# Kernel tuning notes

Hardware: AMD Instinct MI355X
Metric: run time of the kernel (lower is better)

## Reference

```python
import jax, jax.numpy as jnp
import numpy as np

LATENT = 256
HIDDEN = 512
NODE_F = 128
MAX_NODES = 50
B = 128


def _mk_linear(key, fan_in, fan_out):
    kw, kb = jax.random.split(key)
    bound = 1.0 / np.sqrt(fan_in)
    W = jax.random.uniform(kw, (fan_in, fan_out), jnp.float32, -bound, bound)
    b = jax.random.uniform(kb, (fan_out,), jnp.float32, -bound, bound)
    return W, b


def setup_inputs() -> dict:
    key = jax.random.key(0)
    ks = jax.random.split(key, 7)
    z = jax.random.normal(ks[0], (B, LATENT), jnp.float32)
    # node decoder: latent -> hidden -> hidden -> max_nodes*node_features
    nw1, nb1 = _mk_linear(ks[1], LATENT, HIDDEN)
    nw2, nb2 = _mk_linear(ks[2], HIDDEN, HIDDEN)
    nw3, nb3 = _mk_linear(ks[3], HIDDEN, MAX_NODES * NODE_F)
    # edge decoder: latent + 2*node_features -> hidden -> hidden//2 -> 1
    ew1, eb1 = _mk_linear(ks[4], LATENT + 2 * NODE_F, HIDDEN)
    ew2, eb2 = _mk_linear(ks[5], HIDDEN, HIDDEN // 2)
    ew3, eb3 = _mk_linear(ks[6], HIDDEN // 2, 1)
    return {"z": z,
            "nw1": nw1, "nb1": nb1, "nw2": nw2, "nb2": nb2, "nw3": nw3, "nb3": nb3,
            "ew1": ew1, "eb1": eb1, "ew2": ew2, "eb2": eb2, "ew3": ew3, "eb3": eb3}


def reference(z, nw1, nb1, nw2, nb2, nw3, nb3, ew1, eb1, ew2, eb2, ew3, eb3):
    # ---- node decoder ----
    h = jax.nn.relu(z @ nw1 + nb1)
    h = jax.nn.relu(h @ nw2 + nb2)
    node_logits = h @ nw3 + nb3                      # [B, MAX_NODES*NODE_F]
    node_feats = node_logits.reshape(z.shape[0], MAX_NODES, NODE_F)
    node_probs = jax.nn.sigmoid(node_feats)

    # ---- edge decoder: vectorize the O(N^2) python loop over upper-tri pairs ----
    # jnp.triu_indices matches the torch loop order: i ascending, j ascending per i.
    ii, jj = jnp.triu_indices(MAX_NODES, k=1)        # [P] each, P = 1225
    ni = node_feats[:, ii, :]                        # [B, P, NODE_F]
    nj = node_feats[:, jj, :]                        # [B, P, NODE_F]
    zb = jnp.broadcast_to(z[:, None, :], (z.shape[0], ii.shape[0], z.shape[1]))
    edge_in = jnp.concatenate([zb, ni, nj], axis=-1)  # [B, P, LATENT+2*NODE_F]
    e = jax.nn.relu(edge_in @ ew1 + eb1)             # [B, P, HIDDEN]
    e = jax.nn.relu(e @ ew2 + eb2)                   # [B, P, HIDDEN//2]
    edge_probs = jax.nn.sigmoid(e @ ew3 + eb3)[..., 0]  # [B, P]
    return node_probs, edge_probs
```

## Files before the change

### kernel.cpp

```cpp
#include <hip/hip_runtime.h>
#include <hip/hip_bf16.h>
#include <math.h>

#define LATENT 256
#define HIDDEN 512
#define NODE_F 128
#define MAX_NODES 50
#define NPAIRS 1225
#define BATCH 128
#define NODE_OUT 6400
#define MTILE 64
#define TPB 10
#define NBLK 256

typedef __attribute__((ext_vector_type(8))) short short8;
typedef __attribute__((ext_vector_type(4))) float float4v;

union S8U { short8 s; unsigned int u[4]; };

__device__ __forceinline__ float bf2f(ushort u) {
    union { unsigned int i; float f; } v; v.i = ((unsigned int)u) << 16; return v.f;
}
__device__ __forceinline__ ushort f2bf(float f) {
    union { unsigned int i; float f; } v; v.f = f;
    unsigned int r = v.i + 0x7fffu + ((v.i >> 16) & 1u);
    return (ushort)(r >> 16);
}
__device__ __forceinline__ unsigned int pk_bf16(float f0, float f1) {
    __hip_bfloat162 p = __float22bfloat162_rn(float2{f0, f1});
    unsigned int w; __builtin_memcpy(&w, &p, 4); return w;
}
__device__ __forceinline__ float sigmoidf(float x) {
    return 1.0f / (1.0f + __expf(-x));
}

#define TR3_B0   0
#define EW2_B0   800
#define WIU_B0   832
#define WIV_B0   848
#define ZC_B0    864
#define ND_B0    1120
#define PT_B0    1376
#define PREPK_NB 1381

__global__ __launch_bounds__(256) void k_prep_all(
    const float* __restrict__ nw3, ushort* __restrict__ nw3T,
    const float* __restrict__ ew1, const float* __restrict__ ew2,
    ushort* __restrict__ ew2T, ushort* __restrict__ wijT,
    const float* __restrict__ z, const float* __restrict__ eb1,
    float* __restrict__ Zc,
    const float* __restrict__ nw1, const float* __restrict__ nb1,
    const float* __restrict__ nw2, const float* __restrict__ nb2,
    ushort* __restrict__ h2b, int* __restrict__ ptab)
{
    __shared__ float smem[64 * 65];
    int b = blockIdx.x;
    int tid = threadIdx.x;
    int tx = tid & 63, ty = tid >> 6;

    if (b < EW2_B0) {
        int bb = b - TR3_B0;
        int k0 = (bb & 7) * 64;
        int n0 = (bb >> 3) * 64;
#pragma unroll
        for (int r = 0; r < 16; r++) {
            int row = r * 4 + ty;
            smem[row * 65 + tx] = nw3[(k0 + row) * NODE_OUT + n0 + tx];
        }
        __syncthreads();
#pragma unroll
        for (int c = 0; c < 16; c++) {
            int n = c * 4 + ty;
            nw3T[(size_t)(n0 + n) * HIDDEN + k0 + tx] = f2bf(smem[tx * 65 + n]);
        }
    } else if (b < WIU_B0) {
        int bb = b - EW2_B0;
        int k0 = (bb >> 2) * 64;
        int n0 = (bb & 3) * 64;
#pragma unroll
        for (int r = 0; r < 16; r++) {
            int row = r * 4 + ty;
            smem[row * 65 + tx] = ew2[(k0 + row) * 256 + n0 + tx];
        }
        __syncthreads();
#pragma unroll
        for (int c = 0; c < 16; c++) {
            int n = c * 4 + ty;
            ew2T[(n0 + n) * HIDDEN + k0 + tx] = f2bf(smem[tx * 65 + n]);
        }
    } else if (b < WIV_B0) {
        int bb = b - WIU_B0;
        int k0 = (bb >> 3) * 64;
        int n0 = (bb & 7) * 64;
#pragma unroll
        for (int r = 0; r < 16; r++) {
            int row = r * 4 + ty;
            smem[row * 65 + tx] = ew1[(256 + k0 + row) * 512 + n0 + tx];
        }
        __syncthreads();
#pragma unroll
        for (int c = 0; c < 16; c++) {
            int n = c * 4 + ty;
            wijT[(n0 + n) * NODE_F + k0 + tx] = f2bf(smem[tx * 65 + n]);
        }
    } else if (b < ZC_B0) {
        int bb = b - WIV_B0;
        int k0 = (bb >> 3) * 64;
        int n0 = (bb & 7) * 64;
#pragma unroll
        for (int r = 0; r < 16; r++) {
            int row = r * 4 + ty;
            smem[row * 65 + tx] = ew1[(384 + k0 + row) * 512 + n0 + tx];
        }
        __syncthreads();
#pragma unroll
        for (int c = 0; c < 16; c++) {
            int n = c * 4 + ty;
            wijT[(512 + n0 + n) * NODE_F + k0 + tx] = f2bf(smem[tx * 65 + n]);
        }
    } else if (b < ND_B0) {
        int b2 = b - ZC_B0;
        int r = b2 >> 1, o = (b2 & 1) * 256 + tid;
        float* zs = smem;
        zs[tid] = z[r * LATENT + tid];
        __syncthreads();
        float acc = 0.f;
#pragma unroll 8
        for (int k = 0; k < LATENT; k++) acc += zs[k] * ew1[k * HIDDEN + o];
        Zc[r * HIDDEN + o] = acc + eb1[o];
    } else if (b < PT_B0) {
        int b2 = b - ND_B0;
        int r = b2 >> 1, half = b2 & 1;
        float* zs = smem;
        float* hs = smem + 256;
        zs[tid] = z[r * LATENT + tid];
        __syncthreads();
        float a0 = 0.f, a1 = 0.f;
#pragma unroll 8
        for (int k = 0; k < LATENT; k++) {
            float zk = zs[k];
            a0 += zk * nw1[k * HIDDEN + tid];
            a1 += zk * nw1[k * HIDDEN + tid + 256];
        }
        hs[tid]       = fmaxf(a0 + nb1[tid], 0.f);
        hs[tid + 256] = fmaxf(a1 + nb1[tid + 256], 0.f);
        __syncthreads();
        int o = half * 256 + tid;
        float acc = 0.f;
#pragma unroll 8
        for (int k = 0; k < HIDDEN; k++) acc += hs[k] * nw2[k * HIDDEN + o];
        acc += nb2[o];
        h2b[r * HIDDEN + o] = f2bf(fmaxf(acc, 0.f));
    } else {
        int p = (b - PT_B0) * 256 + tid;
        if (p < NPAIRS) {
            int i = 0, off = 0;
            while (p - off >= MAX_NODES - 1 - i) { off += MAX_NODES - 1 - i; ++i; }
            int j = i + 1 + (p - off);
            ptab[p] = (i << 8) | j;
        }
    }
}

__global__ __launch_bounds__(256, 4) void k_node_out_mfma(
    const ushort* __restrict__ h2b, const ushort* __restrict__ nw3T,
    const float* __restrict__ nb3, float* __restrict__ node_probs,
    ushort* __restrict__ node_feats)
{
    int tid = threadIdx.x;
    int wave = tid >> 6, lane = tid & 63;
    int m16 = lane & 15, quad = lane >> 4;
    int n0 = (blockIdx.x >> 1) * 64;
    int m0 = (blockIdx.x & 1) * 64;
    int col = n0 + wave * 16 + m16;

    float4v acc[4];
#pragma unroll
    for (int mt = 0; mt < 4; mt++) acc[mt] = (float4v)(0.f);

    const ushort* bb = nw3T + (size_t)col * HIDDEN;
#pragma unroll
    for (int it = 0; it < 16; ++it) {
        int kk = it * 32 + quad * 8;
        short8 b = *(const short8*)(bb + kk);
#pragma unroll
        for (int mt = 0; mt < 4; mt++) {
            short8 a = *(const short8*)(h2b + (m0 + mt * 16 + m16) * HIDDEN + kk);
            acc[mt] = __builtin_amdgcn_mfma_f32_16x16x32_bf16(a, b, acc[mt], 0, 0, 0);
        }
    }
    float bias = nb3[col];
#pragma unroll
    for (int mt = 0; mt < 4; mt++)
#pragma unroll
        for (int t = 0; t < 4; t++) {
            int row = m0 + mt * 16 + quad * 4 + t;
            float v = acc[mt][t] + bias;
            node_probs[(size_t)row * NODE_OUT + col] = sigmoidf(v);
            node_feats[(size_t)row * NODE_OUT + col] = f2bf(v);
        }
}

__global__ __launch_bounds__(256, 4) void k_uv(
    const ushort* __restrict__ nf, const ushort* __restrict__ wijT,
    ushort* __restrict__ UV)
{
    int tid = threadIdx.x;
    int wave = tid >> 6, lane = tid & 63;
    int m16 = lane & 15, quad = lane >> 4;
    int bm = blockIdx.x >> 2, bn = blockIdx.x & 3;
    int base = bn * 256 + wave * 64;
    int r0 = bm * 64;

    float4v acc[4][4];
#pragma unroll
    for (int mt = 0; mt < 4; mt++)
#pragma unroll
        for (int nt = 0; nt < 4; nt++) acc[mt][nt] = (float4v)(0.f);

#pragma unroll
    for (int k0 = 0; k0 < NODE_F; k0 += 32) {
        int kk = k0 + quad * 8;
        short8 a0 = *(const short8*)(nf + (r0 + m16) * NODE_F + kk);
        short8 a1 = *(const short8*)(nf + (r0 + 16 + m16) * NODE_F + kk);
        short8 a2 = *(const short8*)(nf + (r0 + 32 + m16) * NODE_F + kk);
        short8 a3 = *(const short8*)(nf + (r0 + 48 + m16) * NODE_F + kk);
#pragma unroll
        for (int nt = 0; nt < 4; nt++) {
            int n = base + nt * 16 + m16;
            short8 b = *(const short8*)(wijT + n * NODE_F + kk);
            acc[0][nt] = __builtin_amdgcn_mfma_f32_16x16x32_bf16(a0, b, acc[0][nt], 0, 0, 0);
            acc[1][nt] = __builtin_amdgcn_mfma_f32_16x16x32_bf16(a1, b, acc[1][nt], 0, 0, 0);
            acc[2][nt] = __builtin_amdgcn_mfma_f32_16x16x32_bf16(a2, b, acc[2][nt], 0, 0, 0);
            acc[3][nt] = __builtin_amdgcn_mfma_f32_16x16x32_bf16(a3, b, acc[3][nt], 0, 0, 0);
        }
    }
#pragma unroll
    for (int nt = 0; nt < 4; nt++) {
        int colg = base + nt * 16 + m16;
#pragma unroll
        for (int mt = 0; mt < 4; mt++)
#pragma unroll
            for (int t = 0; t < 4; t++) {
                int rr = r0 + mt * 16 + quad * 4 + t;
                UV[(size_t)rr * 1024 + colg] = f2bf(acc[mt][nt][t]);
            }
    }
}

__global__ __launch_bounds__(512, 2) void k_edge8(
    const float* __restrict__ Zc, const ushort* __restrict__ UV,
    const ushort* __restrict__ ew2T, const float* __restrict__ ew3,
    const float* __restrict__ eb2, const float* __restrict__ eb3,
    const int* __restrict__ ptab, float* __restrict__ out_edges)
{
    __shared__ __align__(16) ushort h1[2][MTILE][HIDDEN + 8];
    __shared__ float part[2][MTILE][33];
    __shared__ int uo5[TPB][MTILE], vo5[TPB][MTILE];

    int tid  = threadIdx.x;
    int blk  = blockIdx.x;
    int b    = blk >> 1;
    int ti0  = (blk & 1) * TPB;

    if (tid < MTILE) {
#pragma unroll
        for (int t = 0; t < TPB; t++) {
            int p = (ti0 + t) * MTILE + tid;
            if (p >= NPAIRS) p = NPAIRS - 1;
            int ij = ptab[p];
            uo5[t][tid] = (b * MAX_NODES + (ij >> 8)) * 1024;
            vo5[t][tid] = (b * MAX_NODES + (ij & 255)) * 1024 + 512;
        }
    }

    int wave = tid >> 6, lane = tid & 63;
    int m16 = lane & 15, quad = lane >> 4;
    int c8 = lane * 8;
    int kk0 = quad * 8;

    float4v zA = *(const float4v*)(Zc + b * HIDDEN + c8);
    float4v zB = *(const float4v*)(Zc + b * HIDDEN + c8 + 4);

    const ushort* bb0 = ew2T + (wave * 32 + m16) * HIDDEN;
    const ushort* bb1 = ew2T + (wave * 32 + 16 + m16) * HIDDEN;
    short8 Breg[16][2];
#pragma unroll
    for (int kc = 0; kc < 16; kc++) {
        Breg[kc][0] = *(const short8*)(bb0 + kc * 32 + kk0);
        Breg[kc][1] = *(const short8*)(bb1 + kc * 32 + kk0);
    }
    float eb2v[2], ew3v[2];
    eb2v[0] = eb2[wave * 32 + m16];      eb2v[1] = eb2[wave * 32 + 16 + m16];
    ew3v[0] = ew3[wave * 32 + m16];      ew3v[1] = ew3[wave * 32 + 16 + m16];

    __syncthreads();

#pragma unroll
    for (int rr = 0; rr < 8; rr++) {
        int r = wave * 8 + rr;
        short8 u8 = *(const short8*)(UV + uo5[0][r] + c8);
        short8 v8 = *(const short8*)(UV + vo5[0][r] + c8);
        S8U hh;
#pragma unroll
        for (int e2 = 0; e2 < 4; e2++) {
            float z0 = (e2 < 2) ? zA[e2 * 2] : zB[e2 * 2 - 4];
            float z1 = (e2 < 2) ? zA[e2 * 2 + 1] : zB[e2 * 2 - 3];
            float f0 = fmaxf(z0 + bf2f((ushort)u8[e2 * 2]) + bf2f((ushort)v8[e2 * 2]), 0.f);
            float f1 = fmaxf(z1 + bf2f((ushort)u8[e2 * 2 + 1]) + bf2f((ushort)v8[e2 * 2 + 1]), 0.f);
            hh.u[e2] = pk_bf16(f0, f1);
        }
        *(short8*)&h1[0][r][c8] = hh.s;
    }
    __syncthreads();

    for (int t = 0; t < TPB; t++) {
        int cur = t & 1, nxt = cur ^ 1;
        bool hasNext = (t + 1 < TPB);

        if (t > 0 && tid < MTILE) {
            int p = (ti0 + t - 1) * MTILE + tid;
            if (p < NPAIRS) {
                float v = eb3[0];
#pragma unroll
                for (int w = 0; w < 32; w++) v += part[nxt][tid][w];
                out_edges[b * NPAIRS + p] = sigmoidf(v);
            }
        }

        float4v acc2[4][2];
#pragma unroll
        for (int mt = 0; mt < 4; mt++)
#pragma unroll
            for (int nt = 0; nt < 2; nt++) acc2[mt][nt] = (float4v)(0.f);

        short8 uu[4], vv[4];
        if (hasNext) {
#pragma unroll
            for (int rr = 0; rr < 4; rr++) {
                int r = wave * 8 + rr;
                uu[rr] = *(const short8*)(UV + uo5[t + 1][r] + c8);
                vv[rr] = *(const short8*)(UV + vo5[t + 1][r] + c8);
            }
        }
#pragma unroll
        for (int it = 0; it < 8; ++it) {
            int kk = it * 32 + kk0;
            short8 a0 = *(const short8*)&h1[cur][m16][kk];
            short8 a1 = *(const short8*)&h1[cur][16 + m16][kk];
            short8 a2 = *(const short8*)&h1[cur][32 + m16][kk];
            short8 a3 = *(const short8*)&h1[cur][48 + m16][kk];
            acc2[0][0] = __builtin_amdgcn_mfma_f32_16x16x32_bf16(a0, Breg[it][0], acc2[0][0], 0, 0, 0);
            acc2[1][0] = __builtin_amdgcn_mfma_f32_16x16x32_bf16(a1, Breg[it][0], acc2[1][0], 0, 0, 0);
            acc2[2][0] = __builtin_amdgcn_mfma_f32_16x16x32_bf16(a2, Breg[it][0], acc2[2][0], 0, 0, 0);
            acc2[3][0] = __builtin_amdgcn_mfma_f32_16x16x32_bf16(a3, Breg[it][0], acc2[3][0], 0, 0, 0);
            acc2[0][1] = __builtin_amdgcn_mfma_f32_16x16x32_bf16(a0, Breg[it][1], acc2[0][1], 0, 0, 0);
            acc2[1][1] = __builtin_amdgcn_mfma_f32_16x16x32_bf16(a1, Breg[it][1], acc2[1][1], 0, 0, 0);
            acc2[2][1] = __builtin_amdgcn_mfma_f32_16x16x32_bf16(a2, Breg[it][1], acc2[2][1], 0, 0, 0);
            acc2[3][1] = __builtin_amdgcn_mfma_f32_16x16x32_bf16(a3, Breg[it][1], acc2[3][1], 0, 0, 0);
        }
        if (hasNext) {
#pragma unroll
            for (int rr = 0; rr < 4; rr++) {
                int r = wave * 8 + rr;
                S8U hh;
#pragma unroll
                for (int e2 = 0; e2 < 4; e2++) {
                    float z0 = (e2 < 2) ? zA[e2 * 2] : zB[e2 * 2 - 4];
                    float z1 = (e2 < 2) ? zA[e2 * 2 + 1] : zB[e2 * 2 - 3];
                    float f0 = fmaxf(z0 + bf2f((ushort)uu[rr][e2 * 2]) + bf2f((ushort)vv[rr][e2 * 2]), 0.f);
                    float f1 = fmaxf(z1 + bf2f((ushort)uu[rr][e2 * 2 + 1]) + bf2f((ushort)vv[rr][e2 * 2 + 1]), 0.f);
                    hh.u[e2] = pk_bf16(f0, f1);
                }
                *(short8*)&h1[nxt][r][c8] = hh.s;
            }
#pragma unroll
            for (int rr = 0; rr < 4; rr++) {
                int r = wave * 8 + 4 + rr;
                uu[rr] = *(const short8*)(UV + uo5[t + 1][r] + c8);
                vv[rr] = *(const short8*)(UV + vo5[t + 1][r] + c8);
            }
        }
#pragma unroll
        for (int it = 8; it < 16; ++it) {
            int kk = it * 32 + kk0;
            short8 a0 = *(const short8*)&h1[cur][m16][kk];
            short8 a1 = *(const short8*)&h1[cur][16 + m16][kk];
            short8 a2 = *(const short8*)&h1[cur][32 + m16][kk];
            short8 a3 = *(const short8*)&h1[cur][48 + m16][kk];
            acc2[0][0] = __builtin_amdgcn_mfma_f32_16x16x32_bf16(a0, Breg[it][0], acc2[0][0], 0, 0, 0);
            acc2[1][0] = __builtin_amdgcn_mfma_f32_16x16x32_bf16(a1, Breg[it][0], acc2[1][0], 0, 0, 0);
            acc2[2][0] = __builtin_amdgcn_mfma_f32_16x16x32_bf16(a2, Breg[it][0], acc2[2][0], 0, 0, 0);
            acc2[3][0] = __builtin_amdgcn_mfma_f32_16x16x32_bf16(a3, Breg[it][0], acc2[3][0], 0, 0, 0);
            acc2[0][1] = __builtin_amdgcn_mfma_f32_16x16x32_bf16(a0, Breg[it][1], acc2[0][1], 0, 0, 0);
            acc2[1][1] = __builtin_amdgcn_mfma_f32_16x16x32_bf16(a1, Breg[it][1], acc2[1][1], 0, 0, 0);
            acc2[2][1] = __builtin_amdgcn_mfma_f32_16x16x32_bf16(a2, Breg[it][1], acc2[2][1], 0, 0, 0);
            acc2[3][1] = __builtin_amdgcn_mfma_f32_16x16x32_bf16(a3, Breg[it][1], acc2[3][1], 0, 0, 0);
        }
        if (hasNext) {
#pragma unroll
            for (int rr = 0; rr < 4; rr++) {
                int r = wave * 8 + 4 + rr;
                S8U hh;
#pragma unroll
                for (int e2 = 0; e2 < 4; e2++) {
                    float z0 = (e2 < 2) ? zA[e2 * 2] : zB[e2 * 2 - 4];
                    float z1 = (e2 < 2) ? zA[e2 * 2 + 1] : zB[e2 * 2 - 3];
                    float f0 = fmaxf(z0 + bf2f((ushort)uu[rr][e2 * 2]) + bf2f((ushort)vv[rr][e2 * 2]), 0.f);
                    float f1 = fmaxf(z1 + bf2f((ushort)uu[rr][e2 * 2 + 1]) + bf2f((ushort)vv[rr][e2 * 2 + 1]), 0.f);
                    hh.u[e2] = pk_bf16(f0, f1);
                }
                *(short8*)&h1[nxt][r][c8] = hh.s;
            }
        }

#pragma unroll
        for (int mt = 0; mt < 4; mt++)
#pragma unroll
            for (int tt = 0; tt < 4; tt++) {
                float s = 0.f;
#pragma unroll
                for (int nt = 0; nt < 2; nt++)
                    s += fmaxf(acc2[mt][nt][tt] + eb2v[nt], 0.f) * ew3v[nt];
                s += __shfl_xor(s, 1);
                s += __shfl_xor(s, 2);
                if ((m16 & 3) == 0)
                    part[cur][mt * 16 + quad * 4 + tt][wave * 4 + (m16 >> 2)] = s;
            }
        __syncthreads();
    }

    if (tid < MTILE) {
        int p = (ti0 + TPB - 1) * MTILE + tid;
        if (p < NPAIRS) {
            float v = eb3[0];
#pragma unroll
            for (int w = 0; w < 32; w++) v += part[(TPB - 1) & 1][tid][w];
            out_edges[b * NPAIRS + p] = sigmoidf(v);
        }
    }
}

extern "C" void kernel_launch(void* const* d_in, const int* in_sizes, int n_in,
                              void* d_out, int out_size, void* d_ws, size_t ws_size,
                              hipStream_t stream) {
    const float* z   = (const float*)d_in[0];
    const float* nw1 = (const float*)d_in[1];
    const float* nb1 = (const float*)d_in[2];
    const float* nw2 = (const float*)d_in[3];
    const float* nb2 = (const float*)d_in[4];
    const float* nw3 = (const float*)d_in[5];
    const float* nb3 = (const float*)d_in[6];
    const float* ew1 = (const float*)d_in[7];
    const float* eb1 = (const float*)d_in[8];
    const float* ew2 = (const float*)d_in[9];
    const float* eb2 = (const float*)d_in[10];
    const float* ew3 = (const float*)d_in[11];
    const float* eb3 = (const float*)d_in[12];

    char* ws = (char*)d_ws;
    int*    ptab = (int*)(ws);
    ushort* h2b  = (ushort*)(ws + 262144);
    ushort* nf   = (ushort*)(ws + 393216);
    ushort* ew2T = (ushort*)(ws + 2031616);
    ushort* wijT = (ushort*)(ws + 2293760);
    ushort* nw3T = (ushort*)(ws + 2555904);
    float*  Zc   = (float*)(ws + 9109504);
    ushort* UV   = (ushort*)(ws + 9371648);

    float* out_nodes = (float*)d_out;
    float* out_edges = out_nodes + BATCH * NODE_OUT;

    k_prep_all<<<PREPK_NB, 256, 0, stream>>>(nw3, nw3T, ew1, ew2, ew2T, wijT,
                                             z, eb1, Zc, nw1, nb1, nw2, nb2,
                                             h2b, ptab);
    k_node_out_mfma<<<200, 256, 0, stream>>>(h2b, nw3T, nb3, out_nodes, nf);
    k_uv<<<400, 256, 0, stream>>>(nf, wijT, UV);
    k_edge8<<<NBLK, 512, 0, stream>>>(Zc, UV, ew2T, ew3, eb2, eb3, ptab, out_edges);
}
```

Measured before the change: 210.9 us.

## Fuse node output GEMM and UV projection into one kernel via LDS

Merges the node-output GEMM and the per-node UV projection into a single kernel. Each block computes a 32-row by 128-column node-feature tile (one node's features for 32 batch rows), stages it in LDS as bf16, and then multiplies it by wijT to produce the 1024-wide UV rows for those batch/node pairs. This removes one launch and the global round trip of the node-feature buffer. In exchange, each block now reads the whole wijT matrix and the grid is only 200 blocks with occupancy bound lowered to 2.

After: 209.2 us (median of 2 runs). No clear change (-0.8%).

```diff
diff --git a/kernel.cpp b/kernel.cpp
--- a/kernel.cpp
+++ b/kernel.cpp
@@ -162,89 +162,85 @@
     }
 }
 
-__global__ __launch_bounds__(256, 4) void k_node_out_mfma(
+__global__ __launch_bounds__(256, 2) void k_node_uv(
     const ushort* __restrict__ h2b, const ushort* __restrict__ nw3T,
-    const float* __restrict__ nb3, float* __restrict__ node_probs,
-    ushort* __restrict__ node_feats)
+    const float* __restrict__ nb3, const ushort* __restrict__ wijT,
+    float* __restrict__ node_probs, ushort* __restrict__ UV)
 {
+    __shared__ ushort nf_lds[32][132];
     int tid = threadIdx.x;
     int wave = tid >> 6, lane = tid & 63;
     int m16 = lane & 15, quad = lane >> 4;
-    int n0 = (blockIdx.x >> 1) * 64;
-    int m0 = (blockIdx.x & 1) * 64;
-    int col = n0 + wave * 16 + m16;
-
-    float4v acc[4];
-#pragma unroll
-    for (int mt = 0; mt < 4; mt++) acc[mt] = (float4v)(0.f);
-
-    const ushort* bb = nw3T + (size_t)col * HIDDEN;
+    int kk0 = quad * 8;
+
+    int nd = blockIdx.x >> 2;
+    int m0 = (blockIdx.x & 3) * 32;
+    int colbase = nd * 128 + wave * 32;
+
+    float4v acc[2][2];
+#pragma unroll
+    for (int mf = 0; mf < 2; mf++)
+#pragma unroll
+        for (int nt = 0; nt < 2; nt++) acc[mf][nt] = (float4v)(0.f);
+
+    const ushort* b0 = nw3T + (size_t)(colbase + m16) * HIDDEN;
+    const ushort* b1 = nw3T + (size_t)(colbase + 16 + m16) * HIDDEN;
+    const ushort* a0p = h2b + (m0 + m16) * HIDDEN;
+    const ushort* a1p = h2b + (m0 + 16 + m16) * HIDDEN;
 #pragma unroll
     for (int it = 0; it < 16; ++it) {
-        int kk = it * 32 + quad * 8;
-        short8 b = *(const short8*)(bb + kk);
-#pragma unroll
-        for (int mt = 0; mt < 4; mt++) {
-            short8 a = *(const short8*)(h2b + (m0 + mt * 16 + m16) * HIDDEN + kk);
-            acc[mt] = __builtin_amdgcn_mfma_f32_16x16x32_bf16(a, b, acc[mt], 0, 0, 0);
-        }
-    }
-    float bias = nb3[col];
-#pragma unroll
-    for (int mt = 0; mt < 4; mt++)
+        int kk = it * 32 + kk0;
+        short8 bf0 = *(const short8*)(b0 + kk);
+        short8 bf1 = *(const short8*)(b1 + kk);
+        short8 af0 = *(const short8*)(a0p + kk);
+        short8 af1 = *(const short8*)(a1p + kk);
+        acc[0][0] = __builtin_amdgcn_mfma_f32_16x16x32_bf16(af0, bf0, acc[0][0], 0, 0, 0);
+        acc[0][1] = __builtin_amdgcn_mfma_f32_16x16x32_bf16(af0, bf1, acc[0][1], 0, 0, 0);
+        acc[1][0] = __builtin_amdgcn_mfma_f32_16x16x32_bf16(af1, bf0, acc[1][0], 0, 0, 0);
+        acc[1][1] = __builtin_amdgcn_mfma_f32_16x16x32_bf16(af1, bf1, acc[1][1], 0, 0, 0);
+    }
+    float bias0 = nb3[colbase + m16];
+    float bias1 = nb3[colbase + 16 + m16];
+#pragma unroll
+    for (int mf = 0; mf < 2; mf++)
+#pragma unroll
+        for (int nt = 0; nt < 2; nt++) {
+            float bias = nt ? bias1 : bias0;
+            int colL = wave * 32 + nt * 16 + m16;
+#pragma unroll
+            for (int t = 0; t < 4; t++) {
+                int rowL = mf * 16 + quad * 4 + t;
+                float v = acc[mf][nt][t] + bias;
+                node_probs[(size_t)(m0 + rowL) * NODE_OUT + nd * 128 + colL] = sigmoidf(v);
+                nf_lds[rowL][colL] = f2bf(v);
+            }
+        }
+    __syncthreads();
+
+    short8 Areg[2][4];
+#pragma unroll
+    for (int mf = 0; mf < 2; mf++)
+#pragma unroll
+        for (int ks = 0; ks < 4; ks++)
+            Areg[mf][ks] = *(const short8*)&nf_lds[mf * 16 + m16][ks * 32 + kk0];
+
+#pragma unroll
+    for (int nfi = 0; nfi < 16; ++nfi) {
+        int colg = wave * 256 + nfi * 16 + m16;
+        const ushort* bp = wijT + colg * NODE_F + kk0;
+        float4v u0 = (float4v)(0.f), u1 = (float4v)(0.f);
+#pragma unroll
+        for (int ks = 0; ks < 4; ks++) {
+            short8 bfr = *(const short8*)(bp + ks * 32);
+            u0 = __builtin_amdgcn_mfma_f32_16x16x32_bf16(Areg[0][ks], bfr, u0, 0, 0, 0);
+            u1 = __builtin_amdgcn_mfma_f32_16x16x32_bf16(Areg[1][ks], bfr, u1, 0, 0, 0);
+        }
 #pragma unroll
         for (int t = 0; t < 4; t++) {
-            int row = m0 + mt * 16 + quad * 4 + t;
-            float v = acc[mt][t] + bias;
-            node_probs[(size_t)row * NODE_OUT + col] = sigmoidf(v);
-            node_feats[(size_t)row * NODE_OUT + col] = f2bf(v);
-        }
-}
-
-__global__ __launch_bounds__(256, 4) void k_uv(
-    const ushort* __restrict__ nf, const ushort* __restrict__ wijT,
-    ushort* __restrict__ UV)
-{
-    int tid = threadIdx.x;
-    int wave = tid >> 6, lane = tid & 63;
-    int m16 = lane & 15, quad = lane >> 4;
-    int bm = blockIdx.x >> 2, bn = blockIdx.x & 3;
-    int base = bn * 256 + wave * 64;
-    int r0 = bm * 64;
-
-    float4v acc[4][4];
-#pragma unroll
-    for (int mt = 0; mt < 4; mt++)
-#pragma unroll
-        for (int nt = 0; nt < 4; nt++) acc[mt][nt] = (float4v)(0.f);
-
-#pragma unroll
-    for (int k0 = 0; k0 < NODE_F; k0 += 32) {
-        int kk = k0 + quad * 8;
-        short8 a0 = *(const short8*)(nf + (r0 + m16) * NODE_F + kk);
-        short8 a1 = *(const short8*)(nf + (r0 + 16 + m16) * NODE_F + kk);
-        short8 a2 = *(const short8*)(nf + (r0 + 32 + m16) * NODE_F + kk);
-        short8 a3 = *(const short8*)(nf + (r0 + 48 + m16) * NODE_F + kk);
-#pragma unroll
-        for (int nt = 0; nt < 4; nt++) {
-            int n = base + nt * 16 + m16;
-            short8 b = *(const short8*)(wijT + n * NODE_F + kk);
-            acc[0][nt] = __builtin_amdgcn_mfma_f32_16x16x32_bf16(a0, b, acc[0][nt], 0, 0, 0);
-            acc[1][nt] = __builtin_amdgcn_mfma_f32_16x16x32_bf16(a1, b, acc[1][nt], 0, 0, 0);
-            acc[2][nt] = __builtin_amdgcn_mfma_f32_16x16x32_bf16(a2, b, acc[2][nt], 0, 0, 0);
-            acc[3][nt] = __builtin_amdgcn_mfma_f32_16x16x32_bf16(a3, b, acc[3][nt], 0, 0, 0);
-        }
-    }
-#pragma unroll
-    for (int nt = 0; nt < 4; nt++) {
-        int colg = base + nt * 16 + m16;
-#pragma unroll
-        for (int mt = 0; mt < 4; mt++)
-#pragma unroll
-            for (int t = 0; t < 4; t++) {
-                int rr = r0 + mt * 16 + quad * 4 + t;
-                UV[(size_t)rr * 1024 + colg] = f2bf(acc[mt][nt][t]);
-            }
+            int r0g = m0 + quad * 4 + t;
+            UV[(size_t)(r0g * MAX_NODES + nd) * 1024 + colg]        = f2bf(u0[t]);
+            UV[(size_t)((r0g + 16) * MAX_NODES + nd) * 1024 + colg] = f2bf(u1[t]);
+        }
     }
 }
 
@@ -461,7 +457,6 @@
     char* ws = (char*)d_ws;
     int*    ptab = (int*)(ws);
     ushort* h2b  = (ushort*)(ws + 262144);
-    ushort* nf   = (ushort*)(ws + 393216);
     ushort* ew2T = (ushort*)(ws + 2031616);
     ushort* wijT = (ushort*)(ws + 2293760);
     ushort* nw3T = (ushort*)(ws + 2555904);
@@ -474,7 +469,6 @@
     k_prep_all<<<PREPK_NB, 256, 0, stream>>>(nw3, nw3T, ew1, ew2, ew2T, wijT,
                                              z, eb1, Zc, nw1, nb1, nw2, nb2,
                                              h2b, ptab);
-    k_node_out_mfma<<<200, 256, 0, stream>>>(h2b, nw3T, nb3, out_nodes, nf);
-    k_uv<<<400, 256, 0, stream>>>(nf, wijT, UV);
+    k_node_uv<<<200, 256, 0, stream>>>(h2b, nw3T, nb3, wijT, out_nodes, UV);
     k_edge8<<<NBLK, 512, 0, stream>>>(Zc, UV, ew2T, ew3, eb2, eb3, ptab, out_edges);
 }
```
